# Kernel tuning notes

Measured on AMD Instinct MI355X. Metric: run time of the kernel, lower is better.

The kernel has to match this reference:

```python
import jax, jax.numpy as jnp
import numpy as np
from jax import lax

DN = ('NCHW', 'OIHW', 'NCHW')


def conv2d(x, w, b, pad):
    y = lax.conv_general_dilated(x, w, (1, 1), [(pad, pad), (pad, pad)], dimension_numbers=DN)
    return y + b[None, :, None, None]


def unfold3x3(x):
    # x: [B, C, H, W] -> [B, C, 9, H, W], matching F.unfold(kernel=3, padding=1)
    B, C, H, W = x.shape
    xp = jnp.pad(x, ((0, 0), (0, 0), (1, 1), (1, 1)))
    views = [xp[:, :, ki:ki + H, kj:kj + W] for ki in range(3) for kj in range(3)]
    return jnp.stack(views, axis=2)


def setup_inputs() -> dict:
    key = jax.random.key(0)
    ks = jax.random.split(key, 4)
    B, C, H, W = 16, 1, 512, 512
    hid, up_h, up_w = 32, 1, 3
    x = jax.random.normal(ks[0], (B, C, H, W), dtype=jnp.float32)
    w1 = jax.random.normal(ks[1], (hid, C, 3, 3), dtype=jnp.float32) * (1.0 / 3.0)
    b1 = jnp.zeros((hid,), dtype=jnp.float32)
    alpha = jnp.full((hid,), 0.25, dtype=jnp.float32)  # PReLU init
    w2 = jax.random.normal(ks[2], (9 * up_h * up_w, hid, 1, 1), dtype=jnp.float32) * (1.0 / np.sqrt(hid))
    b2 = jnp.zeros((9 * up_h * up_w,), dtype=jnp.float32)
    return {"x": x, "target_h": H * up_h, "target_w": W * up_w,
            "w1": w1, "b1": b1, "alpha": alpha, "w2": w2, "b2": b2}


def reference(x, target_h, target_w, w1, b1, alpha, w2, b2):
    B, C, H, W = x.shape
    up_h = target_h // H  # = 1
    up_w = target_w // W  # = 3
    # mask_net: conv3x3 -> PReLU -> conv1x1
    h = conv2d(x, w1, b1, pad=1)
    h = jnp.where(h > 0, h, alpha[None, :, None, None] * h)
    mask = conv2d(h, w2, b2, pad=0)  # [B, 9*up_h*up_w, H, W]
    # convex upsample (anisotropic)
    neigh = unfold3x3(x)  # [B, C, 9, H, W]
    m = mask.reshape(B, 9, up_h, up_w, H, W)
    m = jax.nn.softmax(m, axis=1)
    up = jnp.einsum('bckhw,bkuvhw->bcuvhw', neigh, m)  # [B,C,up_h,up_w,H,W]
    up = up.transpose(0, 1, 4, 2, 5, 3)  # [B,C,H,up_h,W,up_w]
    return up.reshape(B, C, H * up_h, W * up_w)
```

## Files before the change

kernel.cpp:

```cpp
#include <hip/hip_runtime.h>
#include <hip/hip_bf16.h>


#define BB 16
#define HH 512
#define WW 512
#define HID 32
#define NM 27
#define LOG2E 1.44269504088896340736f
#define NT 16384
#define NBLK 1280
#define ROWB 112
#define ZOFF (64 * ROWB)

typedef short bf16x8 __attribute__((ext_vector_type(8)));
typedef float f32x4  __attribute__((ext_vector_type(4)));
typedef unsigned int u32;
typedef u32 u32x4 __attribute__((ext_vector_type(4)));

__device__ __forceinline__ u32 pk2(float a, float b) {
    union { __hip_bfloat162 h2; u32 u; } cv;
    cv.h2 = __float22bfloat162_rn(make_float2(a, b));
    return cv.u;
}

__device__ __forceinline__ void lds_fence() {
    asm volatile("" ::: "memory");
}

__device__ __forceinline__ void load_xv(const float* __restrict__ x, int tile,
                                        int tid, float xv[9]) {
    const int wcol = (tile & 1) * 256 + tid;
    const int hrow = (tile >> 1) & (HH - 1);
    const int bidx = tile >> 10;
    const float* xb = x + (size_t)bidx * (HH * WW);
    int wx[3]; bool wok[3];
#pragma unroll
    for (int i = 0; i < 3; ++i) {
        const int w = wcol + i - 1;
        wok[i] = (unsigned)w < (unsigned)WW;
        wx[i]  = w < 0 ? 0 : (w > WW - 1 ? WW - 1 : w);
    }
#pragma unroll
    for (int ki = 0; ki < 3; ++ki) {
        const int h = hrow + ki - 1;
        const bool hok = (unsigned)h < (unsigned)HH;
        const int hy = h < 0 ? 0 : (h > HH - 1 ? HH - 1 : h);
        const float* rowp = xb + hy * WW;
#pragma unroll
        for (int kj = 0; kj < 3; ++kj) {
            const float v = rowp[wx[kj]];
            xv[ki * 3 + kj] = (hok && wok[kj]) ? v : 0.0f;
        }
    }
}

__global__ void prep_B(const float* __restrict__ w1, const float* __restrict__ b1,
                       const float* __restrict__ alpha, const float* __restrict__ w2,
                       const float* __restrict__ b2, __hip_bfloat16* __restrict__ ws) {
    const int i = blockIdx.x * 256 + threadIdx.x;
    if (i >= 3072) return;
    const int sec = i >> 10;
    const int r   = i & 1023;
    const int n   = r >> 5, k = r & 31;
    float v = 0.0f;
    if (sec == 0) {
        if (n < NM) {
            if (k < 9) {
                for (int c = 0; c < HID; ++c)
                    v += w2[n * HID + c] * (0.5f * (1.0f + alpha[c])) * w1[c * 9 + k];
            } else if (k == 9) {
                v = b2[n];
                for (int c = 0; c < HID; ++c)
                    v += w2[n * HID + c] * (0.5f * (1.0f + alpha[c])) * b1[c];
            }
        }
        v *= LOG2E;
    } else if (sec == 1) {
        if (n < NM) {
            const int c = ((k & 4) ? 16 : 0) + (k >> 3) * 4 + (k & 3);
            v = w2[n * HID + c] * (0.5f * (1.0f - alpha[c])) * LOG2E;
        }
    } else {
        v = (k < 9) ? w1[n * 9 + k] : (k == 9 ? b1[n] : 0.0f);
    }
    ws[i] = __float2bfloat16(v);
}

__global__ __launch_bounds__(256, 5) void convex_upsample_mfma11(
    const float* __restrict__ x,
    const __hip_bfloat16* __restrict__ ws,
    float* __restrict__ out)
{
    __shared__ char lds_raw[4][ZOFF + 16];

    const int tid  = threadIdx.x;
    const int wv   = tid >> 6;
    const int lane = tid & 63;
    const int l16  = lane & 15;
    const int lq   = lane >> 4;
    char* wbase = lds_raw[wv];

    bf16x8 Bf2[2], M2p[2], Bf1[2];
#pragma unroll
    for (int nt = 0; nt < 2; ++nt) {
        const int ro = (nt * 16 + l16) * 32 + lq * 8;
        Bf2[nt] = *(const bf16x8*)(ws + ro);
        M2p[nt] = *(const bf16x8*)(ws + 1024 + ro);
        Bf1[nt] = *(const bf16x8*)(ws + 2048 + ro);
    }

    *(u32x4*)(wbase + ZOFF) = (u32x4){0u, 0u, 0u, 0u};

    int tb = blockIdx.x;
    float xv[9];
    load_xv(x, tb, tid, xv);

    while (tb < NT) {
        const int tn  = tb + NBLK;
        const int tpf = (tn < NT) ? tn : 0;
        float xn[9];
        load_xv(x, tpf, tid, xn);

        char* myrow = wbase + lane * ROWB;
        *(u32x4*)(myrow)      = (u32x4){pk2(xv[0], xv[1]), pk2(xv[2], xv[3]),
                                        pk2(xv[4], xv[5]), pk2(xv[6], xv[7])};
        *(u32x4*)(myrow + 16) = (u32x4){pk2(xv[8], 1.0f), 0u, 0u, 0u};

        lds_fence();

        bf16x8 a0[4];
#pragma unroll
        for (int mt = 0; mt < 4; ++mt) {
            const char* ab = wbase + (mt * 16 + l16) * ROWB;
            const char* aptr = (lq < 2) ? (ab + lq * 16) : (wbase + ZOFF);
            a0[mt] = *(const bf16x8*)aptr;
        }

        lds_fence();

#pragma unroll
        for (int mt = 0; mt < 4; ++mt) {
            char* ab = wbase + (mt * 16 + l16) * ROWB;
            f32x4 z0 = {0.f, 0.f, 0.f, 0.f}, z1 = {0.f, 0.f, 0.f, 0.f};
            z0 = __builtin_amdgcn_mfma_f32_16x16x32_bf16(Bf1[0], a0[mt], z0, 0, 0, 0);
            z1 = __builtin_amdgcn_mfma_f32_16x16x32_bf16(Bf1[1], a0[mt], z1, 0, 0, 0);
            union { u32 u[4]; bf16x8 h; } zf;
            zf.u[0] = pk2(fabsf(z0[0]), fabsf(z0[1]));
            zf.u[1] = pk2(fabsf(z0[2]), fabsf(z0[3]));
            zf.u[2] = pk2(fabsf(z1[0]), fabsf(z1[1]));
            zf.u[3] = pk2(fabsf(z1[2]), fabsf(z1[3]));
            f32x4 c0 = {0.f, 0.f, 0.f, 0.f}, c1 = {0.f, 0.f, 0.f, 0.f};
            c0 = __builtin_amdgcn_mfma_f32_16x16x32_bf16(M2p[0], zf.h,   c0, 0, 0, 0);
            c0 = __builtin_amdgcn_mfma_f32_16x16x32_bf16(Bf2[0], a0[mt], c0, 0, 0, 0);
            c1 = __builtin_amdgcn_mfma_f32_16x16x32_bf16(M2p[1], zf.h,   c1, 0, 0, 0);
            c1 = __builtin_amdgcn_mfma_f32_16x16x32_bf16(Bf2[1], a0[mt], c1, 0, 0, 0);
            *(f32x4*)(ab + 48 + lq * 16) = c0;
            if (lq < 3) *(f32x4*)(ab + lq * 16) = c1;
        }

        lds_fence();

        f32x4 mv[7];
#pragma unroll
        for (int q = 0; q < 4; ++q)
            mv[q] = *(const f32x4*)(myrow + 48 + q * 16);
#pragma unroll
        for (int q = 0; q < 3; ++q)
            mv[4 + q] = *(const f32x4*)(myrow + q * 16);

        const int p = tb * 256 + tid;
        const size_t ob = (size_t)p * 3;
#pragma unroll
        for (int v = 0; v < 3; ++v) {
            float ssum = 0.0f, acc = 0.0f;
#pragma unroll
            for (int k = 0; k < 9; ++k) {
                const int j = k * 3 + v;
                const float lg = (j < 16) ? mv[j >> 2][j & 3]
                                          : mv[4 + ((j - 16) >> 2)][(j - 16) & 3];
                const float e = __builtin_amdgcn_exp2f(lg);
                ssum += e;
                acc = fmaf(xv[k], e, acc);
            }
            out[ob + v] = acc * __builtin_amdgcn_rcpf(ssum);
        }

        lds_fence();

        tb = tn;
#pragma unroll
        for (int k = 0; k < 9; ++k) xv[k] = xn[k];
    }
}

extern "C" void kernel_launch(void* const* d_in, const int* in_sizes, int n_in,
                              void* d_out, int out_size, void* d_ws, size_t ws_size,
                              hipStream_t stream) {
    const float* x     = (const float*)d_in[0];
    const float* w1    = (const float*)d_in[3];
    const float* b1    = (const float*)d_in[4];
    const float* alpha = (const float*)d_in[5];
    const float* w2    = (const float*)d_in[6];
    const float* b2    = (const float*)d_in[7];
    float* out = (float*)d_out;
    __hip_bfloat16* ws = (__hip_bfloat16*)d_ws;

    hipLaunchKernelGGL(prep_B, dim3(12), dim3(256), 0, stream, w1, b1, alpha, w2, b2, ws);
    hipLaunchKernelGGL(convex_upsample_mfma11, dim3(NBLK), dim3(256), 0, stream,
                       x, ws, out);
}
```

Measured before the change: 58.05 us.

## Switch to 32x32x16 MFMA with in-register softmax and cross-half shuffle reduction

Replaces the 16x16x32 MFMA tiling with 32x32x16 bf16 MFMAs. The mask logits stay in accumulator registers instead of round-tripping through LDS, and each half-wave handles part of the 27 logits. The two halves' partial numerators and denominators are then combined with cross-lane shuffles. The weight layout is repacked, and padding rows get a large negative bias so they contribute nothing to the softmax. Grid size and occupancy bounds also change, at the cost of extra shuffles and different register pressure.

New measurement: 58.09 us. No clear change (+0.1%).

```diff
diff --git a/kernel.cpp b/kernel.cpp
--- a/kernel.cpp
+++ b/kernel.cpp
@@ -9,14 +9,15 @@
 #define NM 27
 #define LOG2E 1.44269504088896340736f
 #define NT 16384
-#define NBLK 1280
-#define ROWB 112
-#define ZOFF (64 * ROWB)
+#define NBLK 2048
+#define ROWB 48
 
 typedef short bf16x8 __attribute__((ext_vector_type(8)));
-typedef float f32x4  __attribute__((ext_vector_type(4)));
+typedef float f32x16 __attribute__((ext_vector_type(16)));
 typedef unsigned int u32;
 typedef u32 u32x4 __attribute__((ext_vector_type(4)));
+
+#define ZERO16 (f32x16){0.f,0.f,0.f,0.f,0.f,0.f,0.f,0.f,0.f,0.f,0.f,0.f,0.f,0.f,0.f,0.f}
 
 __device__ __forceinline__ u32 pk2(float a, float b) {
     union { __hip_bfloat162 h2; u32 u; } cv;
@@ -59,58 +60,61 @@
                        const float* __restrict__ alpha, const float* __restrict__ w2,
                        const float* __restrict__ b2, __hip_bfloat16* __restrict__ ws) {
     const int i = blockIdx.x * 256 + threadIdx.x;
-    if (i >= 3072) return;
-    const int sec = i >> 10;
-    const int r   = i & 1023;
-    const int n   = r >> 5, k = r & 31;
+    if (i >= 2048) return;
+    const int sec = i >> 9;
+    const int rr  = i & 511;
+    const int n   = rr >> 4, c = rr & 15;
+    const int lo  = (n >> 2) & 1;
+    const int r   = (n & 3) + 4 * (n >> 3);
+    const bool valid = lo == 0 ? (r < 15) : (r < 12);
+    const int k = (lo == 0) ? (r / 3) : (5 + r / 3);
+    const int j = 3 * k + (r % 3);
+    const int ch = (c & 3) + 8 * ((c >> 2) & 1) + 4 * (c >> 3);
     float v = 0.0f;
     if (sec == 0) {
-        if (n < NM) {
-            if (k < 9) {
-                for (int c = 0; c < HID; ++c)
-                    v += w2[n * HID + c] * (0.5f * (1.0f + alpha[c])) * w1[c * 9 + k];
-            } else if (k == 9) {
-                v = b2[n];
-                for (int c = 0; c < HID; ++c)
-                    v += w2[n * HID + c] * (0.5f * (1.0f + alpha[c])) * b1[c];
+        if (valid) {
+            if (c < 9) {
+                for (int q = 0; q < HID; ++q)
+                    v += w2[j * HID + q] * (0.5f * (1.0f + alpha[q])) * w1[q * 9 + c];
+                v *= LOG2E;
+            } else if (c == 9) {
+                v = b2[j];
+                for (int q = 0; q < HID; ++q)
+                    v += w2[j * HID + q] * (0.5f * (1.0f + alpha[q])) * b1[q];
+                v *= LOG2E;
             }
-        }
-        v *= LOG2E;
+        } else if (c == 9) {
+            v = -100.0f;
+        }
     } else if (sec == 1) {
-        if (n < NM) {
-            const int c = ((k & 4) ? 16 : 0) + (k >> 3) * 4 + (k & 3);
-            v = w2[n * HID + c] * (0.5f * (1.0f - alpha[c])) * LOG2E;
-        }
+        if (valid) v = w2[j * HID + ch] * (0.5f * (1.0f - alpha[ch])) * LOG2E;
+    } else if (sec == 2) {
+        if (valid) v = w2[j * HID + 16 + ch] * (0.5f * (1.0f - alpha[16 + ch])) * LOG2E;
     } else {
-        v = (k < 9) ? w1[n * 9 + k] : (k == 9 ? b1[n] : 0.0f);
+        v = (c < 9) ? w1[n * 9 + c] : (c == 9 ? b1[n] : 0.0f);
     }
     ws[i] = __float2bfloat16(v);
 }
 
-__global__ __launch_bounds__(256, 5) void convex_upsample_mfma11(
+__global__ __launch_bounds__(256, 4) void convex_upsample_w32(
     const float* __restrict__ x,
     const __hip_bfloat16* __restrict__ ws,
     float* __restrict__ out)
 {
-    __shared__ char lds_raw[4][ZOFF + 16];
+    __shared__ char lds_raw[4][64 * ROWB];
 
     const int tid  = threadIdx.x;
     const int wv   = tid >> 6;
     const int lane = tid & 63;
-    const int l16  = lane & 15;
-    const int lq   = lane >> 4;
+    const int l32  = lane & 31;
+    const int lo   = lane >> 5;
     char* wbase = lds_raw[wv];
 
-    bf16x8 Bf2[2], M2p[2], Bf1[2];
-#pragma unroll
-    for (int nt = 0; nt < 2; ++nt) {
-        const int ro = (nt * 16 + l16) * 32 + lq * 8;
-        Bf2[nt] = *(const bf16x8*)(ws + ro);
-        M2p[nt] = *(const bf16x8*)(ws + 1024 + ro);
-        Bf1[nt] = *(const bf16x8*)(ws + 2048 + ro);
-    }
-
-    *(u32x4*)(wbase + ZOFF) = (u32x4){0u, 0u, 0u, 0u};
+    const int widx = l32 * 16 + lo * 8;
+    const bf16x8 B2a  = *(const bf16x8*)(ws + widx);
+    const bf16x8 M2pL = *(const bf16x8*)(ws + 512 + widx);
+    const bf16x8 M2pH = *(const bf16x8*)(ws + 1024 + widx);
+    const bf16x8 B1f  = *(const bf16x8*)(ws + 1536 + widx);
 
     int tb = blockIdx.x;
     float xv[9];
@@ -129,64 +133,63 @@
 
         lds_fence();
 
-        bf16x8 a0[4];
-#pragma unroll
-        for (int mt = 0; mt < 4; ++mt) {
-            const char* ab = wbase + (mt * 16 + l16) * ROWB;
-            const char* aptr = (lq < 2) ? (ab + lq * 16) : (wbase + ZOFF);
-            a0[mt] = *(const bf16x8*)aptr;
-        }
+        const bf16x8 aA = *(const bf16x8*)(wbase + l32 * ROWB + lo * 16);
+        const bf16x8 aB = *(const bf16x8*)(wbase + (32 + l32) * ROWB + lo * 16);
 
         lds_fence();
 
-#pragma unroll
-        for (int mt = 0; mt < 4; ++mt) {
-            char* ab = wbase + (mt * 16 + l16) * ROWB;
-            f32x4 z0 = {0.f, 0.f, 0.f, 0.f}, z1 = {0.f, 0.f, 0.f, 0.f};
-            z0 = __builtin_amdgcn_mfma_f32_16x16x32_bf16(Bf1[0], a0[mt], z0, 0, 0, 0);
-            z1 = __builtin_amdgcn_mfma_f32_16x16x32_bf16(Bf1[1], a0[mt], z1, 0, 0, 0);
-            union { u32 u[4]; bf16x8 h; } zf;
-            zf.u[0] = pk2(fabsf(z0[0]), fabsf(z0[1]));
-            zf.u[1] = pk2(fabsf(z0[2]), fabsf(z0[3]));
-            zf.u[2] = pk2(fabsf(z1[0]), fabsf(z1[1]));
-            zf.u[3] = pk2(fabsf(z1[2]), fabsf(z1[3]));
-            f32x4 c0 = {0.f, 0.f, 0.f, 0.f}, c1 = {0.f, 0.f, 0.f, 0.f};
-            c0 = __builtin_amdgcn_mfma_f32_16x16x32_bf16(M2p[0], zf.h,   c0, 0, 0, 0);
-            c0 = __builtin_amdgcn_mfma_f32_16x16x32_bf16(Bf2[0], a0[mt], c0, 0, 0, 0);
-            c1 = __builtin_amdgcn_mfma_f32_16x16x32_bf16(M2p[1], zf.h,   c1, 0, 0, 0);
-            c1 = __builtin_amdgcn_mfma_f32_16x16x32_bf16(Bf2[1], a0[mt], c1, 0, 0, 0);
-            *(f32x4*)(ab + 48 + lq * 16) = c0;
-            if (lq < 3) *(f32x4*)(ab + lq * 16) = c1;
-        }
-
-        lds_fence();
-
-        f32x4 mv[7];
-#pragma unroll
-        for (int q = 0; q < 4; ++q)
-            mv[q] = *(const f32x4*)(myrow + 48 + q * 16);
-#pragma unroll
-        for (int q = 0; q < 3; ++q)
-            mv[4 + q] = *(const f32x4*)(myrow + q * 16);
-
-        const int p = tb * 256 + tid;
-        const size_t ob = (size_t)p * 3;
+        float xsh[9];
+#pragma unroll
+        for (int i = 0; i < 9; ++i) xsh[i] = __shfl_xor(xv[i], 32, 64);
+        float xsel[2][5];
+#pragma unroll
+        for (int i = 0; i < 4; ++i) {
+            xsel[0][i] = lo ? xsh[5 + i] : xv[i];
+            xsel[1][i] = lo ? xv[5 + i] : xsh[i];
+        }
+        xsel[0][4] = lo ? 0.0f : xv[4];
+        xsel[1][4] = lo ? 0.0f : xsh[4];
+
+        float num[2][3], den[2][3];
+#pragma unroll
+        for (int f = 0; f < 2; ++f) {
+            const bf16x8 a = f ? aB : aA;
+            f32x16 zz = ZERO16;
+            zz = __builtin_amdgcn_mfma_f32_32x32x16_bf16(B1f, a, zz, 0, 0, 0);
+            union { u32 u[8]; bf16x8 h[2]; } zf;
+#pragma unroll
+            for (int i = 0; i < 8; ++i)
+                zf.u[i] = pk2(fabsf(zz[2 * i]), fabsf(zz[2 * i + 1]));
+            f32x16 m = ZERO16;
+            m = __builtin_amdgcn_mfma_f32_32x32x16_bf16(B2a,  a,       m, 0, 0, 0);
+            m = __builtin_amdgcn_mfma_f32_32x32x16_bf16(M2pL, zf.h[0], m, 0, 0, 0);
+            m = __builtin_amdgcn_mfma_f32_32x32x16_bf16(M2pH, zf.h[1], m, 0, 0, 0);
+            float nu[3] = {0.f, 0.f, 0.f}, de[3] = {0.f, 0.f, 0.f};
+#pragma unroll
+            for (int r = 0; r < 15; ++r) {
+                const float e = __builtin_amdgcn_exp2f(m[r]);
+                de[r % 3] += e;
+                nu[r % 3] = fmaf(xsel[f][r / 3], e, nu[r % 3]);
+            }
+#pragma unroll
+            for (int v = 0; v < 3; ++v) { num[f][v] = nu[v]; den[f][v] = de[v]; }
+        }
+
+#pragma unroll
+        for (int f = 0; f < 2; ++f)
+#pragma unroll
+            for (int v = 0; v < 3; ++v) {
+                num[f][v] += __shfl_xor(num[f][v], 32, 64);
+                den[f][v] += __shfl_xor(den[f][v], 32, 64);
+            }
+
+        const size_t ob = (size_t)(tb * 256 + tid) * 3;
 #pragma unroll
         for (int v = 0; v < 3; ++v) {
-            float ssum = 0.0f, acc = 0.0f;
-#pragma unroll
-            for (int k = 0; k < 9; ++k) {
-                const int j = k * 3 + v;
-                const float lg = (j < 16) ? mv[j >> 2][j & 3]
-                                          : mv[4 + ((j - 16) >> 2)][(j - 16) & 3];
-                const float e = __builtin_amdgcn_exp2f(lg);
-                ssum += e;
-                acc = fmaf(xv[k], e, acc);
-            }
-            out[ob + v] = acc * __builtin_amdgcn_rcpf(ssum);
-        }
-
-        lds_fence();
+            const float nn = lo ? num[1][v] : num[0][v];
+            const float dd = lo ? den[1][v] : den[0][v];
+            out[ob + v] = nn * __builtin_amdgcn_rcpf(dd);
+        }
 
         tb = tn;
 #pragma unroll
@@ -206,7 +209,7 @@
     float* out = (float*)d_out;
     __hip_bfloat16* ws = (__hip_bfloat16*)d_ws;
 
-    hipLaunchKernelGGL(prep_B, dim3(12), dim3(256), 0, stream, w1, b1, alpha, w2, b2, ws);
-    hipLaunchKernelGGL(convex_upsample_mfma11, dim3(NBLK), dim3(256), 0, stream,
+    hipLaunchKernelGGL(prep_B, dim3(8), dim3(256), 0, stream, w1, b1, alpha, w2, b2, ws);
+    hipLaunchKernelGGL(convex_upsample_w32, dim3(NBLK), dim3(256), 0, stream,
                        x, ws, out);
 }
```
